# Kernel tuning notes

Hardware: AMD Instinct MI355X
Metric: run time of the kernel (lower is better)

Reference implementation:

```python
import jax, jax.numpy as jnp
import numpy as np

N = 100000
E = 3200000
IN_DIM = 512
OUT_DIM = 128


def setup_inputs() -> dict:
    key = jax.random.key(0)
    k1, k2, k3 = jax.random.split(key, 3)
    x = jax.random.normal(k1, (N, IN_DIM), dtype=jnp.float32)
    edge_index = jax.random.randint(k2, (2, E), 0, N, dtype=jnp.int64)
    # Glorot init like PyG GCNConv
    W = jax.random.normal(k3, (IN_DIM, OUT_DIM), dtype=jnp.float32) * (2.0 / (IN_DIM + OUT_DIM)) ** 0.5
    b = jnp.zeros((OUT_DIM,), dtype=jnp.float32)
    return {"x": x, "edge_index": edge_index, "W": W, "b": b}


def gcn_conv(x, edge_index, W, b):
    # GCNConv with add_self_loops=True, normalize=True (symmetric norm)
    row, col = edge_index[0], edge_index[1]  # messages flow row -> col
    xw = x @ W  # [N, out_dim]
    ones = jnp.ones((E,), dtype=xw.dtype)
    # degree of destination nodes, +1 for self-loop
    deg = jax.ops.segment_sum(ones, col, num_segments=N) + 1.0
    dinv = jax.lax.rsqrt(deg)  # deg^{-1/2}, deg >= 1 so no inf
    norm = dinv[row] * dinv[col]  # [E]
    msg = xw[row] * norm[:, None]  # gather + scale
    out = jax.ops.segment_sum(msg, col, num_segments=N)  # scatter-add
    # self-loop contribution: norm_ii = dinv_i * dinv_i
    out = out + xw * (dinv * dinv)[:, None]
    return out + b


def reference(x, edge_index, W, b):
    return gcn_conv(x, edge_index, W, b)
```

## Files before the change

kernel.cpp:

```cpp
#include <hip/hip_runtime.h>

using short8 = __attribute__((ext_vector_type(8))) short;
using f32x4  = __attribute__((ext_vector_type(4))) float;

static constexpr int N_NODES = 100000;
static constexpr int N_EDGES = 3200000;
static constexpr int IN_DIM  = 512;
static constexpr int OUT_DIM = 128;
static constexpr int NBINS   = (N_NODES + 255) / 256;
static constexpr int NB      = 1024;
static constexpr int CHUNK   = N_EDGES / NB;

__device__ __forceinline__ short f2bf(float f) {
  unsigned u = __builtin_bit_cast(unsigned, f);
  u = (u + 0x7FFFu + ((u >> 16) & 1u)) >> 16;
  return (short)u;
}

__global__ __launch_bounds__(256) void cast_WT(const float* __restrict__ W,
                                               short* __restrict__ WT) {
  const int idx = blockIdx.x * 256 + threadIdx.x;
  const int c = idx >> 9, k = idx & 511;
  WT[(size_t)c * 512 + k] = f2bf(W[(size_t)k * 128 + c]);
}

__global__ __launch_bounds__(256) void gemm_mfma(const float* __restrict__ x,
                                                 const short* __restrict__ WT,
                                                 const float* __restrict__ dinv,
                                                 unsigned short* __restrict__ xwb) {
  __shared__ short As[2][64 * 128];
  const int tid  = threadIdx.x;
  const int row0 = blockIdx.x * 64;

  float4 pf[8];

  auto issue_loads = [&](int kb) {
#pragma unroll
    for (int c = 0; c < 4; ++c) {
      const int flat = c * 2048 + tid * 8;
      const int r = flat >> 7;
      const int k = flat & 127;
      const int row = row0 + r;
      if (row < N_NODES) {
        const float* s = &x[(size_t)row * IN_DIM + kb + k];
        pf[c * 2]     = *reinterpret_cast<const float4*>(s);
        pf[c * 2 + 1] = *reinterpret_cast<const float4*>(s + 4);
      } else {
        pf[c * 2]     = make_float4(0.f, 0.f, 0.f, 0.f);
        pf[c * 2 + 1] = make_float4(0.f, 0.f, 0.f, 0.f);
      }
    }
  };

  auto write_lds = [&](int buf) {
#pragma unroll
    for (int c = 0; c < 4; ++c) {
      const int flat = c * 2048 + tid * 8;
      const int r = flat >> 7;
      const int k = flat & 127;
      const float4 f0 = pf[c * 2], f1 = pf[c * 2 + 1];
      short8 sv;
      sv[0] = f2bf(f0.x); sv[1] = f2bf(f0.y); sv[2] = f2bf(f0.z); sv[3] = f2bf(f0.w);
      sv[4] = f2bf(f1.x); sv[5] = f2bf(f1.y); sv[6] = f2bf(f1.z); sv[7] = f2bf(f1.w);
      const int byte = (k * 2) ^ ((r & 7) << 4);
      *reinterpret_cast<short8*>(reinterpret_cast<char*>(As[buf]) + r * 256 + byte) = sv;
    }
  };

  const int l  = tid & 63;
  const int w  = tid >> 6;
  const int wr = w >> 1, wc = w & 1;
  const int lr = l & 15;
  const int lk = l >> 4;

  const int arow0 = wr * 32 + lr;
  const int arow1 = arow0 + 16;
  const int ab0 = arow0 * 256, rx0 = (arow0 & 7) << 4;
  const int ab1 = arow1 * 256, rx1 = (arow1 & 7) << 4;

  const short* bB0 = WT + (size_t)(wc * 64 +  0 + lr) * 512 + lk * 8;
  const short* bB1 = WT + (size_t)(wc * 64 + 16 + lr) * 512 + lk * 8;
  const short* bB2 = WT + (size_t)(wc * 64 + 32 + lr) * 512 + lk * 8;
  const short* bB3 = WT + (size_t)(wc * 64 + 48 + lr) * 512 + lk * 8;

  f32x4 acc[2][4] = {};

  issue_loads(0);
  write_lds(0);
  __syncthreads();

#pragma unroll
  for (int kbidx = 0; kbidx < 4; ++kbidx) {
    const int cur = kbidx & 1;
    if (kbidx < 3) issue_loads((kbidx + 1) * 128);

    const char* base = reinterpret_cast<const char*>(As[cur]);
#pragma unroll
    for (int ks = 0; ks < 4; ++ks) {
      const int kbyte = ks * 64 + lk * 16;
      const short8 a0 = *reinterpret_cast<const short8*>(base + ab0 + (kbyte ^ rx0));
      const short8 a1 = *reinterpret_cast<const short8*>(base + ab1 + (kbyte ^ rx1));
      const int ko = kbidx * 128 + ks * 32;
      const short8 bb0 = *reinterpret_cast<const short8*>(bB0 + ko);
      const short8 bb1 = *reinterpret_cast<const short8*>(bB1 + ko);
      const short8 bb2 = *reinterpret_cast<const short8*>(bB2 + ko);
      const short8 bb3 = *reinterpret_cast<const short8*>(bB3 + ko);
      acc[0][0] = __builtin_amdgcn_mfma_f32_16x16x32_bf16(a0, bb0, acc[0][0], 0, 0, 0);
      acc[0][1] = __builtin_amdgcn_mfma_f32_16x16x32_bf16(a0, bb1, acc[0][1], 0, 0, 0);
      acc[0][2] = __builtin_amdgcn_mfma_f32_16x16x32_bf16(a0, bb2, acc[0][2], 0, 0, 0);
      acc[0][3] = __builtin_amdgcn_mfma_f32_16x16x32_bf16(a0, bb3, acc[0][3], 0, 0, 0);
      acc[1][0] = __builtin_amdgcn_mfma_f32_16x16x32_bf16(a1, bb0, acc[1][0], 0, 0, 0);
      acc[1][1] = __builtin_amdgcn_mfma_f32_16x16x32_bf16(a1, bb1, acc[1][1], 0, 0, 0);
      acc[1][2] = __builtin_amdgcn_mfma_f32_16x16x32_bf16(a1, bb2, acc[1][2], 0, 0, 0);
      acc[1][3] = __builtin_amdgcn_mfma_f32_16x16x32_bf16(a1, bb3, acc[1][3], 0, 0, 0);
    }

    if (kbidx < 3) {
      write_lds(cur ^ 1);
      __syncthreads();
    }
  }

#pragma unroll
  for (int m = 0; m < 2; ++m) {
    const int rbase = row0 + wr * 32 + m * 16 + (l >> 4) * 4;
#pragma unroll
    for (int j = 0; j < 4; ++j) {
      const int row = rbase + j;
      if (row < N_NODES) {
        const float sc = dinv[row];
        unsigned short* o = &xwb[(size_t)row * OUT_DIM + wc * 64 + lr];
        o[0]  = (unsigned short)f2bf(acc[m][0][j] * sc);
        o[16] = (unsigned short)f2bf(acc[m][1][j] * sc);
        o[32] = (unsigned short)f2bf(acc[m][2][j] * sc);
        o[48] = (unsigned short)f2bf(acc[m][3][j] * sc);
      }
    }
  }
}


__global__ __launch_bounds__(256) void bin_count(const int* __restrict__ ecol,
                                                 int* __restrict__ blkhist) {
  __shared__ int hist[NBINS];
  const int blk = blockIdx.x, tid = threadIdx.x;
  for (int i = tid; i < NBINS; i += 256) hist[i] = 0;
  __syncthreads();
  const int e0 = blk * CHUNK, e1 = e0 + CHUNK;
  for (int e = e0 + tid; e < e1; e += 256) atomicAdd(&hist[ecol[e] >> 8], 1);
  __syncthreads();
  for (int i = tid; i < NBINS; i += 256) blkhist[(size_t)blk * NBINS + i] = hist[i];
}

__global__ __launch_bounds__(1024) void scan_blkhist(int* __restrict__ blkhist,
                                                     int* __restrict__ bintot) {
  __shared__ int sh[NB];
  const int bin = blockIdx.x, t = threadIdx.x;
  const int v = blkhist[(size_t)t * NBINS + bin];
  sh[t] = v;
  __syncthreads();
  for (int d = 1; d < NB; d <<= 1) {
    const int tv = (t >= d) ? sh[t - d] : 0;
    __syncthreads();
    sh[t] += tv;
    __syncthreads();
  }
  blkhist[(size_t)t * NBINS + bin] = sh[t] - v;
  if (t == NB - 1) bintot[bin] = sh[t];
}

__global__ __launch_bounds__(512) void scan_bins(const int* __restrict__ bintot,
                                                 int* __restrict__ binbase) {
  __shared__ int sh[512];
  const int t = threadIdx.x;
  const int v = (t < NBINS) ? bintot[t] : 0;
  sh[t] = v;
  __syncthreads();
  for (int d = 1; d < 512; d <<= 1) {
    const int tv = (t >= d) ? sh[t - d] : 0;
    __syncthreads();
    sh[t] += tv;
    __syncthreads();
  }
  if (t < NBINS) binbase[t] = sh[t] - v;
  if (t == NBINS - 1) binbase[NBINS] = sh[t];
}

__global__ __launch_bounds__(256) void bin_scatter(const int* __restrict__ erow,
                                                   const int* __restrict__ ecol,
                                                   const int* __restrict__ blkhist,
                                                   const int* __restrict__ binbase,
                                                   unsigned* __restrict__ benc) {
  __shared__ int cur[NBINS];
  const int blk = blockIdx.x, tid = threadIdx.x;
  for (int i = tid; i < NBINS; i += 256)
    cur[i] = binbase[i] + blkhist[(size_t)blk * NBINS + i];
  __syncthreads();
  const int e0 = blk * CHUNK, e1 = e0 + CHUNK;
  for (int e = e0 + tid; e < e1; e += 256) {
    const int c = ecol[e];
    const unsigned enc = (unsigned)erow[e] | ((unsigned)(c & 255) << 24);
    const int p = atomicAdd(&cur[c >> 8], 1);
    benc[p] = enc;
  }
}

__global__ __launch_bounds__(256) void bin_build(const unsigned* __restrict__ benc,
                                                 const int* __restrict__ binbase,
                                                 int* __restrict__ brow,
                                                 int* __restrict__ offs,
                                                 float* __restrict__ dinv) {
  __shared__ int hist[256];
  __shared__ int sh[256];
  __shared__ int cur[256];
  const int b = blockIdx.x, tid = threadIdx.x;
  const int e0 = binbase[b], e1 = binbase[b + 1];
  hist[tid] = 0;
  __syncthreads();
  for (int e = e0 + tid; e < e1; e += 256) atomicAdd(&hist[benc[e] >> 24], 1);
  __syncthreads();
  const int d0 = hist[tid];
  sh[tid] = d0;
  __syncthreads();
  for (int d = 1; d < 256; d <<= 1) {
    const int tv = (tid >= d) ? sh[tid - d] : 0;
    __syncthreads();
    sh[tid] += tv;
    __syncthreads();
  }
  const int myoff = e0 + sh[tid] - d0;
  cur[tid] = myoff;
  const int node = (b << 8) + tid;
  if (node < N_NODES) {
    offs[node] = myoff;
    dinv[node] = rsqrtf((float)d0 + 1.0f);
  }
  if (b == NBINS - 1 && tid == 255) offs[N_NODES] = e1;
  __syncthreads();
  for (int e = e0 + tid; e < e1; e += 256) {
    const unsigned v = benc[e];
    const int p = atomicAdd(&cur[v >> 24], 1);
    brow[p] = (int)(v & 0x00FFFFFFu);
  }
}

__global__ __launch_bounds__(256) void gather_out(const unsigned short* __restrict__ xwb,
                                                  const float* __restrict__ dinv,
                                                  const int* __restrict__ offs,
                                                  const int* __restrict__ brow,
                                                  const float* __restrict__ bias,
                                                  float* __restrict__ out) {
  const int lane = threadIdx.x & 63;
  const int node = blockIdx.x * (blockDim.x >> 6) + (threadIdx.x >> 6);
  if (node >= N_NODES) return;
  const float di = dinv[node];
  const int c0 = lane * 2;

  auto ld2 = [&](int r) -> float2 {
    const unsigned v = *reinterpret_cast<const unsigned*>(&xwb[(size_t)r * OUT_DIM + c0]);
    float2 f;
    f.x = __builtin_bit_cast(float, v << 16);
    f.y = __builtin_bit_cast(float, v & 0xFFFF0000u);
    return f;
  };

  float2 acc = ld2(node);

  int e = offs[node];
  const int e1 = offs[node + 1];
  for (; e + 8 <= e1; e += 8) {
    const int r0 = brow[e],     r1 = brow[e + 1], r2 = brow[e + 2], r3 = brow[e + 3];
    const int r4 = brow[e + 4], r5 = brow[e + 5], r6 = brow[e + 6], r7 = brow[e + 7];
    const float2 v0 = ld2(r0), v1 = ld2(r1), v2 = ld2(r2), v3 = ld2(r3);
    const float2 v4 = ld2(r4), v5 = ld2(r5), v6 = ld2(r6), v7 = ld2(r7);
    acc.x += ((v0.x + v1.x) + (v2.x + v3.x)) + ((v4.x + v5.x) + (v6.x + v7.x));
    acc.y += ((v0.y + v1.y) + (v2.y + v3.y)) + ((v4.y + v5.y) + (v6.y + v7.y));
  }
  for (; e < e1; ++e) {
    const float2 v = ld2(brow[e]);
    acc.x += v.x;
    acc.y += v.y;
  }

  const float2 bb = *reinterpret_cast<const float2*>(&bias[c0]);
  float2 o;
  o.x = acc.x * di + bb.x;
  o.y = acc.y * di + bb.y;
  *reinterpret_cast<float2*>(&out[(size_t)node * OUT_DIM + c0]) = o;
}

extern "C" void kernel_launch(void* const* d_in, const int* in_sizes, int n_in,
                              void* d_out, int out_size, void* d_ws, size_t ws_size,
                              hipStream_t stream) {
  const float* x    = (const float*)d_in[0];
  const int*   eidx = (const int*)d_in[1];
  const float* W    = (const float*)d_in[2];
  const float* b    = (const float*)d_in[3];
  float* out = (float*)d_out;

  const int* erow = eidx;
  const int* ecol = eidx + N_EDGES;

  char* ws = (char*)d_ws;
  size_t off = 0;
  auto alloc = [&](size_t bytes) -> void* {
    void* p = ws + off;
    off = (off + bytes + 255) & ~(size_t)255;
    return p;
  };
  unsigned short* xwb = (unsigned short*)alloc((size_t)N_NODES * OUT_DIM * sizeof(short));
  short* WT      = (short*)alloc((size_t)OUT_DIM * IN_DIM * sizeof(short));
  float* dinv    = (float*)alloc((size_t)N_NODES * sizeof(float));
  int*   offs    = (int*)alloc((size_t)(N_NODES + 1) * sizeof(int));
  int*   blkhist = (int*)alloc((size_t)NB * NBINS * sizeof(int));
  int*   bintot  = (int*)alloc((size_t)NBINS * sizeof(int));
  int*   binbase = (int*)alloc((size_t)(NBINS + 1) * sizeof(int));
  int*   brow    = (int*)alloc((size_t)N_EDGES * sizeof(int));
  unsigned* benc = (unsigned*)alloc((size_t)N_EDGES * sizeof(unsigned));

  cast_WT<<<256, 256, 0, stream>>>(W, WT);

  bin_count<<<NB, 256, 0, stream>>>(ecol, blkhist);
  scan_blkhist<<<NBINS, NB, 0, stream>>>(blkhist, bintot);
  scan_bins<<<1, 512, 0, stream>>>(bintot, binbase);
  bin_scatter<<<NB, 256, 0, stream>>>(erow, ecol, blkhist, binbase, benc);
  bin_build<<<NBINS, 256, 0, stream>>>(benc, binbase, brow, offs, dinv);

  gemm_mfma<<<(N_NODES + 63) / 64, 256, 0, stream>>>(x, WT, dinv, xwb);
  gather_out<<<(N_NODES + 3) / 4, 256, 0, stream>>>(xwb, dinv, offs, brow, b, out);
}
```

Baseline: 302.1 us.

## Deepen GEMM prefetch pipeline with smaller K tiles and two register stages

The GEMM K tile shrinks from 128 to 64, halving LDS per buffer, and two register prefetch stages are kept so global loads are issued two tiles ahead of compute. The aim is to hide global memory latency for the x stream better and possibly raise occupancy through the smaller LDS footprint. In exchange there are twice as many barriers, and register pressure stays roughly the same.

```diff
diff --git a/kernel.cpp b/kernel.cpp
--- a/kernel.cpp
+++ b/kernel.cpp
@@ -28,18 +28,18 @@
                                                  const short* __restrict__ WT,
                                                  const float* __restrict__ dinv,
                                                  unsigned short* __restrict__ xwb) {
-  __shared__ short As[2][64 * 128];
+  __shared__ short As[2][64 * 64];
   const int tid  = threadIdx.x;
   const int row0 = blockIdx.x * 64;
 
-  float4 pf[8];
-
-  auto issue_loads = [&](int kb) {
-#pragma unroll
-    for (int c = 0; c < 4; ++c) {
+  float4 pf0[4], pf1[4];
+
+  auto issue = [&](int kb, float4* pf) {
+#pragma unroll
+    for (int c = 0; c < 2; ++c) {
       const int flat = c * 2048 + tid * 8;
-      const int r = flat >> 7;
-      const int k = flat & 127;
+      const int r = flat >> 6;
+      const int k = flat & 63;
       const int row = row0 + r;
       if (row < N_NODES) {
         const float* s = &x[(size_t)row * IN_DIM + kb + k];
@@ -52,18 +52,18 @@
     }
   };
 
-  auto write_lds = [&](int buf) {
-#pragma unroll
-    for (int c = 0; c < 4; ++c) {
+  auto wlds = [&](const float4* pf, int buf) {
+#pragma unroll
+    for (int c = 0; c < 2; ++c) {
       const int flat = c * 2048 + tid * 8;
-      const int r = flat >> 7;
-      const int k = flat & 127;
+      const int r = flat >> 6;
+      const int k = flat & 63;
       const float4 f0 = pf[c * 2], f1 = pf[c * 2 + 1];
       short8 sv;
       sv[0] = f2bf(f0.x); sv[1] = f2bf(f0.y); sv[2] = f2bf(f0.z); sv[3] = f2bf(f0.w);
       sv[4] = f2bf(f1.x); sv[5] = f2bf(f1.y); sv[6] = f2bf(f1.z); sv[7] = f2bf(f1.w);
       const int byte = (k * 2) ^ ((r & 7) << 4);
-      *reinterpret_cast<short8*>(reinterpret_cast<char*>(As[buf]) + r * 256 + byte) = sv;
+      *reinterpret_cast<short8*>(reinterpret_cast<char*>(As[buf]) + r * 128 + byte) = sv;
     }
   };
 
@@ -75,8 +75,8 @@
 
   const int arow0 = wr * 32 + lr;
   const int arow1 = arow0 + 16;
-  const int ab0 = arow0 * 256, rx0 = (arow0 & 7) << 4;
-  const int ab1 = arow1 * 256, rx1 = (arow1 & 7) << 4;
+  const int ab0 = arow0 * 128, rx0 = (arow0 & 7) << 4;
+  const int ab1 = arow1 * 128, rx1 = (arow1 & 7) << 4;
 
   const short* bB0 = WT + (size_t)(wc * 64 +  0 + lr) * 512 + lk * 8;
   const short* bB1 = WT + (size_t)(wc * 64 + 16 + lr) * 512 + lk * 8;
@@ -85,22 +85,14 @@
 
   f32x4 acc[2][4] = {};
 
-  issue_loads(0);
-  write_lds(0);
-  __syncthreads();
-
-#pragma unroll
-  for (int kbidx = 0; kbidx < 4; ++kbidx) {
-    const int cur = kbidx & 1;
-    if (kbidx < 3) issue_loads((kbidx + 1) * 128);
-
-    const char* base = reinterpret_cast<const char*>(As[cur]);
-#pragma unroll
-    for (int ks = 0; ks < 4; ++ks) {
+  auto compute = [&](int buf, int kbidx) {
+    const char* base = reinterpret_cast<const char*>(As[buf]);
+#pragma unroll
+    for (int ks = 0; ks < 2; ++ks) {
       const int kbyte = ks * 64 + lk * 16;
       const short8 a0 = *reinterpret_cast<const short8*>(base + ab0 + (kbyte ^ rx0));
       const short8 a1 = *reinterpret_cast<const short8*>(base + ab1 + (kbyte ^ rx1));
-      const int ko = kbidx * 128 + ks * 32;
+      const int ko = kbidx * 64 + ks * 32;
       const short8 bb0 = *reinterpret_cast<const short8*>(bB0 + ko);
       const short8 bb1 = *reinterpret_cast<const short8*>(bB1 + ko);
       const short8 bb2 = *reinterpret_cast<const short8*>(bB2 + ko);
@@ -114,12 +106,21 @@
       acc[1][2] = __builtin_amdgcn_mfma_f32_16x16x32_bf16(a1, bb2, acc[1][2], 0, 0, 0);
       acc[1][3] = __builtin_amdgcn_mfma_f32_16x16x32_bf16(a1, bb3, acc[1][3], 0, 0, 0);
     }
-
-    if (kbidx < 3) {
-      write_lds(cur ^ 1);
-      __syncthreads();
-    }
-  }
+  };
+
+  issue(0, pf0);
+  issue(64, pf1);
+  wlds(pf0, 0);
+  __syncthreads();
+
+  compute(0, 0); issue(128, pf0); wlds(pf1, 1); __syncthreads();
+  compute(1, 1); issue(192, pf1); wlds(pf0, 0); __syncthreads();
+  compute(0, 2); issue(256, pf0); wlds(pf1, 1); __syncthreads();
+  compute(1, 3); issue(320, pf1); wlds(pf0, 0); __syncthreads();
+  compute(0, 4); issue(384, pf0); wlds(pf1, 1); __syncthreads();
+  compute(1, 5); issue(448, pf1); wlds(pf0, 0); __syncthreads();
+  compute(0, 6); wlds(pf1, 1); __syncthreads();
+  compute(1, 7);
 
 #pragma unroll
   for (int m = 0; m < 2; ++m) {
```

Result: no change. 299.7 us (-0.8%).

## Replace LDS-staged GEMM with direct register-fed MFMA over all output columns

Applied to the files above, without the earlier changes.

Rewrites the x@W GEMM so that each wave loads its own 32 rows of x straight from global memory into registers in MFMA fragment layout, converts them to bf16 in place, and computes all 128 output columns. This removes the shared-memory staging, the swizzled LDS writes and the block barriers, and avoids loading each x row twice across the column-split waves. In exchange each wave reloads W fragments from global/L2 for every k-step, register pressure rises with 16 accumulators, and the x loads are less coalesced because each lane reads a 32-byte strip.

```diff
diff --git a/kernel.cpp b/kernel.cpp
--- a/kernel.cpp
+++ b/kernel.cpp
@@ -24,116 +24,73 @@
   WT[(size_t)c * 512 + k] = f2bf(W[(size_t)k * 128 + c]);
 }
 
-__global__ __launch_bounds__(256) void gemm_mfma(const float* __restrict__ x,
-                                                 const short* __restrict__ WT,
-                                                 const float* __restrict__ dinv,
-                                                 unsigned short* __restrict__ xwb) {
-  __shared__ short As[2][64 * 128];
-  const int tid  = threadIdx.x;
-  const int row0 = blockIdx.x * 64;
-
-  float4 pf[8];
-
-  auto issue_loads = [&](int kb) {
-#pragma unroll
-    for (int c = 0; c < 4; ++c) {
-      const int flat = c * 2048 + tid * 8;
-      const int r = flat >> 7;
-      const int k = flat & 127;
-      const int row = row0 + r;
-      if (row < N_NODES) {
-        const float* s = &x[(size_t)row * IN_DIM + kb + k];
-        pf[c * 2]     = *reinterpret_cast<const float4*>(s);
-        pf[c * 2 + 1] = *reinterpret_cast<const float4*>(s + 4);
-      } else {
-        pf[c * 2]     = make_float4(0.f, 0.f, 0.f, 0.f);
-        pf[c * 2 + 1] = make_float4(0.f, 0.f, 0.f, 0.f);
-      }
+__global__ __launch_bounds__(256) void gemm_direct(const float* __restrict__ x,
+                                                   const short* __restrict__ WT,
+                                                   const float* __restrict__ dinv,
+                                                   unsigned short* __restrict__ xwb) {
+  const int tid = threadIdx.x;
+  const int w   = tid >> 6;
+  const int l   = tid & 63;
+  const int lr  = l & 15;
+  const int lk  = l >> 4;
+  const int row0 = blockIdx.x * 128 + w * 32;
+
+  const int ra = min(row0 + lr, N_NODES - 1);
+  const int rb = min(row0 + 16 + lr, N_NODES - 1);
+  const float* pa = &x[(size_t)ra * IN_DIM + lk * 8];
+  const float* pb = &x[(size_t)rb * IN_DIM + lk * 8];
+  const short* wbase = WT + (size_t)lr * 512 + lk * 8;
+
+  f32x4 acc[2][8] = {};
+
+  float4 a00 = *reinterpret_cast<const float4*>(pa);
+  float4 a01 = *reinterpret_cast<const float4*>(pa + 4);
+  float4 a10 = *reinterpret_cast<const float4*>(pb);
+  float4 a11 = *reinterpret_cast<const float4*>(pb + 4);
+
+#pragma unroll
+  for (int ks = 0; ks < 16; ++ks) {
+    float4 n00, n01, n10, n11;
+    if (ks < 15) {
+      const float* qa = pa + (ks + 1) * 32;
+      const float* qb = pb + (ks + 1) * 32;
+      n00 = *reinterpret_cast<const float4*>(qa);
+      n01 = *reinterpret_cast<const float4*>(qa + 4);
+      n10 = *reinterpret_cast<const float4*>(qb);
+      n11 = *reinterpret_cast<const float4*>(qb + 4);
     }
-  };
-
-  auto write_lds = [&](int buf) {
-#pragma unroll
-    for (int c = 0; c < 4; ++c) {
-      const int flat = c * 2048 + tid * 8;
-      const int r = flat >> 7;
-      const int k = flat & 127;
-      const float4 f0 = pf[c * 2], f1 = pf[c * 2 + 1];
-      short8 sv;
-      sv[0] = f2bf(f0.x); sv[1] = f2bf(f0.y); sv[2] = f2bf(f0.z); sv[3] = f2bf(f0.w);
-      sv[4] = f2bf(f1.x); sv[5] = f2bf(f1.y); sv[6] = f2bf(f1.z); sv[7] = f2bf(f1.w);
-      const int byte = (k * 2) ^ ((r & 7) << 4);
-      *reinterpret_cast<short8*>(reinterpret_cast<char*>(As[buf]) + r * 256 + byte) = sv;
+
+    short8 bb[8];
+#pragma unroll
+    for (int cf = 0; cf < 8; ++cf)
+      bb[cf] = *reinterpret_cast<const short8*>(wbase + (size_t)cf * 16 * 512 + ks * 32);
+
+    short8 a0, a1;
+    a0[0] = f2bf(a00.x); a0[1] = f2bf(a00.y); a0[2] = f2bf(a00.z); a0[3] = f2bf(a00.w);
+    a0[4] = f2bf(a01.x); a0[5] = f2bf(a01.y); a0[6] = f2bf(a01.z); a0[7] = f2bf(a01.w);
+    a1[0] = f2bf(a10.x); a1[1] = f2bf(a10.y); a1[2] = f2bf(a10.z); a1[3] = f2bf(a10.w);
+    a1[4] = f2bf(a11.x); a1[5] = f2bf(a11.y); a1[6] = f2bf(a11.z); a1[7] = f2bf(a11.w);
+
+#pragma unroll
+    for (int cf = 0; cf < 8; ++cf) {
+      acc[0][cf] = __builtin_amdgcn_mfma_f32_16x16x32_bf16(a0, bb[cf], acc[0][cf], 0, 0, 0);
+      acc[1][cf] = __builtin_amdgcn_mfma_f32_16x16x32_bf16(a1, bb[cf], acc[1][cf], 0, 0, 0);
     }
-  };
-
-  const int l  = tid & 63;
-  const int w  = tid >> 6;
-  const int wr = w >> 1, wc = w & 1;
-  const int lr = l & 15;
-  const int lk = l >> 4;
-
-  const int arow0 = wr * 32 + lr;
-  const int arow1 = arow0 + 16;
-  const int ab0 = arow0 * 256, rx0 = (arow0 & 7) << 4;
-  const int ab1 = arow1 * 256, rx1 = (arow1 & 7) << 4;
-
-  const short* bB0 = WT + (size_t)(wc * 64 +  0 + lr) * 512 + lk * 8;
-  const short* bB1 = WT + (size_t)(wc * 64 + 16 + lr) * 512 + lk * 8;
-  const short* bB2 = WT + (size_t)(wc * 64 + 32 + lr) * 512 + lk * 8;
-  const short* bB3 = WT + (size_t)(wc * 64 + 48 + lr) * 512 + lk * 8;
-
-  f32x4 acc[2][4] = {};
-
-  issue_loads(0);
-  write_lds(0);
-  __syncthreads();
-
-#pragma unroll
-  for (int kbidx = 0; kbidx < 4; ++kbidx) {
-    const int cur = kbidx & 1;
-    if (kbidx < 3) issue_loads((kbidx + 1) * 128);
-
-    const char* base = reinterpret_cast<const char*>(As[cur]);
-#pragma unroll
-    for (int ks = 0; ks < 4; ++ks) {
-      const int kbyte = ks * 64 + lk * 16;
-      const short8 a0 = *reinterpret_cast<const short8*>(base + ab0 + (kbyte ^ rx0));
-      const short8 a1 = *reinterpret_cast<const short8*>(base + ab1 + (kbyte ^ rx1));
-      const int ko = kbidx * 128 + ks * 32;
-      const short8 bb0 = *reinterpret_cast<const short8*>(bB0 + ko);
-      const short8 bb1 = *reinterpret_cast<const short8*>(bB1 + ko);
-      const short8 bb2 = *reinterpret_cast<const short8*>(bB2 + ko);
-      const short8 bb3 = *reinterpret_cast<const short8*>(bB3 + ko);
-      acc[0][0] = __builtin_amdgcn_mfma_f32_16x16x32_bf16(a0, bb0, acc[0][0], 0, 0, 0);
-      acc[0][1] = __builtin_amdgcn_mfma_f32_16x16x32_bf16(a0, bb1, acc[0][1], 0, 0, 0);
-      acc[0][2] = __builtin_amdgcn_mfma_f32_16x16x32_bf16(a0, bb2, acc[0][2], 0, 0, 0);
-      acc[0][3] = __builtin_amdgcn_mfma_f32_16x16x32_bf16(a0, bb3, acc[0][3], 0, 0, 0);
-      acc[1][0] = __builtin_amdgcn_mfma_f32_16x16x32_bf16(a1, bb0, acc[1][0], 0, 0, 0);
-      acc[1][1] = __builtin_amdgcn_mfma_f32_16x16x32_bf16(a1, bb1, acc[1][1], 0, 0, 0);
-      acc[1][2] = __builtin_amdgcn_mfma_f32_16x16x32_bf16(a1, bb2, acc[1][2], 0, 0, 0);
-      acc[1][3] = __builtin_amdgcn_mfma_f32_16x16x32_bf16(a1, bb3, acc[1][3], 0, 0, 0);
-    }
-
-    if (kbidx < 3) {
-      write_lds(cur ^ 1);
-      __syncthreads();
-    }
+
+    a00 = n00; a01 = n01; a10 = n10; a11 = n11;
   }
 
 #pragma unroll
   for (int m = 0; m < 2; ++m) {
-    const int rbase = row0 + wr * 32 + m * 16 + (l >> 4) * 4;
 #pragma unroll
     for (int j = 0; j < 4; ++j) {
-      const int row = rbase + j;
+      const int row = row0 + m * 16 + lk * 4 + j;
       if (row < N_NODES) {
         const float sc = dinv[row];
-        unsigned short* o = &xwb[(size_t)row * OUT_DIM + wc * 64 + lr];
-        o[0]  = (unsigned short)f2bf(acc[m][0][j] * sc);
-        o[16] = (unsigned short)f2bf(acc[m][1][j] * sc);
-        o[32] = (unsigned short)f2bf(acc[m][2][j] * sc);
-        o[48] = (unsigned short)f2bf(acc[m][3][j] * sc);
+        unsigned short* o = &xwb[(size_t)row * OUT_DIM + lr];
+#pragma unroll
+        for (int cf = 0; cf < 8; ++cf)
+          o[cf * 16] = (unsigned short)f2bf(acc[m][cf][j] * sc);
       }
     }
   }
@@ -326,6 +283,6 @@
   bin_scatter<<<NB, 256, 0, stream>>>(erow, ecol, blkhist, binbase, benc);
   bin_build<<<NBINS, 256, 0, stream>>>(benc, binbase, brow, offs, dinv);
 
-  gemm_mfma<<<(N_NODES + 63) / 64, 256, 0, stream>>>(x, WT, dinv, xwb);
+  gemm_direct<<<(N_NODES + 127) / 128, 256, 0, stream>>>(x, WT, dinv, xwb);
   gather_out<<<(N_NODES + 3) / 4, 256, 0, stream>>>(xwb, dinv, offs, brow, b, out);
 }
```

New measurement: 331.0 us. 1.1x slower.
